# Performance work log

Hardware: AMD Instinct MI355X
Metric: run time of the kernel (lower is better)

Reference implementation:

```python
import jax, jax.numpy as jnp
import numpy as np
from jax import lax

B, M, D_IN, EPG = 512, 64, 32, 512   # pairs, nodes/graph, one_hot_dim, edges/graph
GCN_SIZES = [64, 32, 16]
K = 5                                 # conv kernel (odd -> 'same' pad 2)
LIN = [12288, 256, 64]                # 12288 = 3 sim-mats * 16 ch * 16 * 16


def _edges(seed):
    # random intra-graph edges: per-graph node ids in [0,M) offset by graph id
    r = np.random.default_rng(seed)
    off = np.repeat(np.arange(B, dtype=np.int64) * M, EPG)
    s = r.integers(0, M, B * EPG) + off
    d = r.integers(0, M, B * EPG) + off
    return jnp.asarray(s, jnp.int32), jnp.asarray(d, jnp.int32)


def setup_inputs():
    key = jax.random.key(0)
    ks = iter(jax.random.split(key, 32))
    def nrm(shape, fan_in):
        return jax.random.normal(next(ks), shape, jnp.float32) * (fan_in ** -0.5)
    src_q, dst_q = _edges(1)
    src_c, dst_c = _edges(2)
    return dict(
        x_q=jax.random.normal(next(ks), (B * M, D_IN), jnp.float32),
        x_c=jax.random.normal(next(ks), (B * M, D_IN), jnp.float32),
        src_q=src_q, dst_q=dst_q, src_c=src_c, dst_c=dst_c,
        Wg0=nrm((D_IN, 64), D_IN), bg0=jnp.zeros((64,), jnp.float32),
        Wg1=nrm((64, 32), 64), bg1=jnp.zeros((32,), jnp.float32),
        Wg2=nrm((32, 16), 32), bg2=jnp.zeros((16,), jnp.float32),
        cw0=nrm((3, 8, 1, K, K), K * K), cb0=jnp.zeros((3, 8), jnp.float32),
        cw1=nrm((3, 16, 8, K, K), 8 * K * K), cb1=jnp.zeros((3, 16), jnp.float32),
        Wl0=nrm((LIN[0], LIN[1]), LIN[0]), bl0=jnp.zeros((LIN[1],), jnp.float32),
        Wl1=nrm((LIN[1], LIN[2]), LIN[1]), bl1=jnp.zeros((LIN[2],), jnp.float32),
        Wsc=nrm((LIN[2], 1), LIN[2]), bsc=jnp.zeros((1,), jnp.float32),
    )


def _gcn_pass(x, src, dst, Ws, bs):
    # PyG GCNConv: x @ W, add self loops, symmetric deg^-1/2 normalization,
    # scatter-add to dst, + bias. Eval mode (dropout off).
    N = x.shape[0]
    sl = jnp.arange(N, dtype=src.dtype)
    s = jnp.concatenate([src, sl])
    d = jnp.concatenate([dst, sl])
    deg = jax.ops.segment_sum(jnp.ones(s.shape, x.dtype), d, num_segments=N)
    dinv = lax.rsqrt(deg)
    norm = (dinv[s] * dinv[d])[:, None]
    feats = []
    h = x
    for i in range(len(Ws)):
        h = h @ Ws[i]
        h = jax.ops.segment_sum(h[s] * norm, d, num_segments=N) + bs[i]
        feats.append(h)
        if i < len(Ws) - 1:
            h = jax.nn.relu(h)
    return feats


def _conv(x, w, b):
    y = lax.conv_general_dilated(x, w, (1, 1), ((K // 2, K // 2), (K // 2, K // 2)),
                                 dimension_numbers=('NCHW', 'OIHW', 'NCHW'))
    return y + b[None, :, None, None]


def _maxpool2(x):
    # torch: ZeroPad2d((0,1,0,1)) then MaxPool2d(2, 2)
    xp = jnp.pad(x, ((0, 0), (0, 0), (0, 1), (0, 1)))
    return lax.reduce_window(xp, -jnp.inf, lax.max, (1, 1, 2, 2), (1, 1, 2, 2), 'VALID')


def _forward(x_q, x_c, src_q, dst_q, src_c, dst_c,
             Wg0, bg0, Wg1, bg1, Wg2, bg2,
             cw0, cb0, cw1, cb1, Wl0, bl0, Wl1, bl1, Wsc, bsc):
    Ws, bs = [Wg0, Wg1, Wg2], [bg0, bg1, bg2]
    qf = _gcn_pass(x_q, src_q, dst_q, Ws, bs)
    cf = _gcn_pass(x_c, src_c, dst_c, Ws, bs)
    # all graphs have exactly M nodes -> pad_sequence is a reshape; sim is [B,1,M,M]
    feats = [jnp.einsum('bmd,bnd->bmn', qf[i].reshape(B, M, -1),
                        cf[i].reshape(B, M, -1))[:, None] for i in range(3)]
    cws, cbs = [cw0, cw1], [cb0, cb1]
    for l in range(2):
        feats = [_maxpool2(jax.nn.relu(_conv(feats[i], cws[l][i], cbs[l][i])))
                 for i in range(3)]
    h = jnp.concatenate(feats, axis=1).reshape(-1, LIN[0])
    h = jax.nn.relu(h @ Wl0 + bl0)
    h = jax.nn.relu(h @ Wl1 + bl1)
    return jax.nn.sigmoid(h @ Wsc + bsc).reshape(-1)


def reference(x_q, x_c, src_q, dst_q, src_c, dst_c,
              Wg0, bg0, Wg1, bg1, Wg2, bg2,
              cw0, cb0, cw1, cb1, Wl0, bl0, Wl1, bl1, Wsc, bsc):
    return _forward(x_q, x_c, src_q, dst_q, src_c, dst_c,
                    Wg0, bg0, Wg1, bg1, Wg2, bg2,
                    cw0, cb0, cw1, cb1, Wl0, bl0, Wl1, bl1, Wsc, bsc)
```

## Files before the change

kernel.cpp:

```cpp
#include <hip/hip_runtime.h>
#include <math.h>

#define NB 512
#define MM 64
#define EPGc 512

typedef __attribute__((ext_vector_type(8))) short s16x8;
typedef __attribute__((ext_vector_type(4))) float f32x4;

__device__ __forceinline__ unsigned short f2bf(float f) {
  union { float f; unsigned int u; } c; c.f = f;
  unsigned int u = c.u;
  return (unsigned short)((u + 0x7FFFu + ((u >> 16) & 1u)) >> 16);
}
__device__ __forceinline__ float bf2f(unsigned short h) {
  union { unsigned int u; float f; } c; c.u = ((unsigned int)h) << 16;
  return c.f;
}

template<int Fin, int Fout, bool RELU>
__device__ __forceinline__ void gcn_layer_mfma(
    const unsigned short* __restrict__ WT, const float* __restrict__ bias,
    unsigned short* hbuf, unsigned short* stT, const unsigned short* Ab,
    unsigned short* __restrict__ outG, int g, int tid)
{
  const int lane = tid & 63, w = tid >> 6;
  const int c = lane & 15, q = lane >> 4;
  constexpr int NT = Fout / 16;
  constexpr int KS = Fin / 32;

#pragma unroll
  for (int nt = 0; nt < NT; ++nt) {
    f32x4 acc = {0.f, 0.f, 0.f, 0.f};
#pragma unroll
    for (int ks = 0; ks < KS; ++ks) {
      s16x8 a = *reinterpret_cast<const s16x8*>(hbuf + (w * 16 + c) * 72 + ks * 32 + q * 8);
      s16x8 b = *reinterpret_cast<const s16x8*>(WT + (nt * 16 + c) * Fin + ks * 32 + q * 8);
      acc = __builtin_amdgcn_mfma_f32_16x16x32_bf16(a, b, acc, 0, 0, 0);
    }
    unsigned int w0 = (unsigned int)f2bf(acc[0]) | ((unsigned int)f2bf(acc[1]) << 16);
    unsigned int w1 = (unsigned int)f2bf(acc[2]) | ((unsigned int)f2bf(acc[3]) << 16);
    *reinterpret_cast<uint2*>(stT + (nt * 16 + c) * 72 + w * 16 + q * 4) = make_uint2(w0, w1);
  }
  __syncthreads();

#pragma unroll
  for (int mt = 0; mt < NT; ++mt) {
    f32x4 acc = {0.f, 0.f, 0.f, 0.f};
#pragma unroll
    for (int ks = 0; ks < 2; ++ks) {
      s16x8 a = *reinterpret_cast<const s16x8*>(stT + (mt * 16 + c) * 72 + ks * 32 + q * 8);
      s16x8 b = *reinterpret_cast<const s16x8*>(Ab + (w * 16 + c) * 72 + ks * 32 + q * 8);
      acc = __builtin_amdgcn_mfma_f32_16x16x32_bf16(a, b, acc, 0, 0, 0);
    }
    const int node = w * 16 + c, f0 = mt * 16 + q * 4;
    unsigned short pk[4], pr[4];
#pragma unroll
    for (int r = 0; r < 4; ++r) {
      float v = acc[r] + bias[f0 + r];
      pk[r] = f2bf(v);
      pr[r] = f2bf(fmaxf(v, 0.f));
    }
    *reinterpret_cast<uint2*>(outG + (size_t)(g * MM + node) * Fout + f0) =
        make_uint2((unsigned int)pk[0] | ((unsigned int)pk[1] << 16),
                   (unsigned int)pk[2] | ((unsigned int)pk[3] << 16));
    if (RELU)
      *reinterpret_cast<uint2*>(hbuf + node * 72 + f0) =
          make_uint2((unsigned int)pr[0] | ((unsigned int)pr[1] << 16),
                     (unsigned int)pr[2] | ((unsigned int)pr[3] << 16));
  }
  __syncthreads();
}

__global__ __launch_bounds__(256) void gcn_kernel(
    const float* __restrict__ xq, const float* __restrict__ xc,
    const int* __restrict__ srcq, const int* __restrict__ dstq,
    const int* __restrict__ srcc, const int* __restrict__ dstc,
    const unsigned short* __restrict__ WgT,
    const float* __restrict__ bg0, const float* __restrict__ bg1, const float* __restrict__ bg2,
    unsigned short* __restrict__ qf0, unsigned short* __restrict__ qf1,
    unsigned short* __restrict__ qf2, unsigned short* __restrict__ cf0,
    unsigned short* __restrict__ cf1, unsigned short* __restrict__ cf2)
{
  __shared__ __align__(16) unsigned short smem[13824];
  __shared__ float sDinv[MM];
  __shared__ int sDeg[MM];
  unsigned short* hbuf = smem;
  unsigned short* stT  = smem + 4608;
  unsigned short* Ab   = smem + 9216;
  float* sAf = reinterpret_cast<float*>(smem);

  const int g = blockIdx.x;
  const int which = blockIdx.y;
  const float* x = which ? xc : xq;
  const int* src = which ? srcc : srcq;
  const int* dst = which ? dstc : dstq;
  unsigned short* f0p = which ? cf0 : qf0;
  unsigned short* f1p = which ? cf1 : qf1;
  unsigned short* f2p = which ? cf2 : qf2;
  const int tid = threadIdx.x;

  for (int i = tid; i < 64 * 68; i += 256) sAf[i] = 0.f;
  if (tid < MM) sDeg[tid] = 1;
  __syncthreads();
  for (int e = tid; e < EPGc; e += 256)
    atomicAdd(&sDeg[dst[g * EPGc + e] - g * MM], 1);
  __syncthreads();
  if (tid < MM) sDinv[tid] = rsqrtf((float)sDeg[tid]);
  __syncthreads();
  for (int e = tid; e < EPGc; e += 256) {
    int s = src[g * EPGc + e] - g * MM;
    int d = dst[g * EPGc + e] - g * MM;
    atomicAdd(&sAf[d * 68 + s], sDinv[s] * sDinv[d]);
  }
  if (tid < MM) atomicAdd(&sAf[tid * 68 + tid], sDinv[tid] * sDinv[tid]);
  __syncthreads();
  for (int i = tid; i < 4096; i += 256) {
    int r = i >> 6, s = i & 63;
    Ab[r * 72 + s] = f2bf(sAf[r * 68 + s]);
  }
  __syncthreads();
  {
    const float* xs = x + (size_t)g * 2048 + tid * 8;
    float4 v0 = *reinterpret_cast<const float4*>(xs);
    float4 v1 = *reinterpret_cast<const float4*>(xs + 4);
    s16x8 p;
    p[0] = (short)f2bf(v0.x); p[1] = (short)f2bf(v0.y); p[2] = (short)f2bf(v0.z); p[3] = (short)f2bf(v0.w);
    p[4] = (short)f2bf(v1.x); p[5] = (short)f2bf(v1.y); p[6] = (short)f2bf(v1.z); p[7] = (short)f2bf(v1.w);
    int node = tid >> 2, k = (tid & 3) * 8;
    *reinterpret_cast<s16x8*>(hbuf + node * 72 + k) = p;
  }
  __syncthreads();

  gcn_layer_mfma<32, 64, true >(WgT,        bg0, hbuf, stT, Ab, f0p, g, tid);
  gcn_layer_mfma<64, 32, true >(WgT + 2048, bg1, hbuf, stT, Ab, f1p, g, tid);
  gcn_layer_mfma<32, 16, false>(WgT + 4096, bg2, hbuf, stT, Ab, f2p, g, tid);
}

__global__ __launch_bounds__(256) void prep_misc(
    const float* __restrict__ cw1, const float* __restrict__ cw0,
    const float* __restrict__ bl0,
    const float* __restrict__ Wg0, const float* __restrict__ Wg1, const float* __restrict__ Wg2,
    unsigned short* __restrict__ packA, unsigned short* __restrict__ packW1,
    unsigned short* __restrict__ WgT, float* __restrict__ l0)
{
  const int b = blockIdx.x, t = threadIdx.x;
  if (b < 512) {
    l0[b * 256 + t] = bl0[t];
    return;
  }
  if (b < 554) {
    int i = (b - 512) * 256 + t;
    if (i < 10752) {
      int j = i & 7, l = (i >> 3) & 63, g = (i >> 9) % 7, lvl = i / 3584;
      int oc = l & 15, sg = l >> 4;
      int s = g * 4 + sg;
      float v = 0.f;
      if (s < 25) v = cw1[((size_t)(lvl * 16 + oc) * 8 + j) * 25 + s];
      packA[i] = f2bf(v);
    }
    return;
  }
  if (b < 566) {
    int i = (b - 554) * 256 + t;
    if (i < 3072) {
      int j = i & 7, lane = (i >> 3) & 63, gg = (i >> 9) & 1, lvl = i >> 10;
      int m = lane & 15, q = lane >> 4;
      int u = gg * 4 + q;
      int oc = m & 7;
      float v = 0.f;
      if (u < 5) {
        if (m < 8) { if (j < 5) v = cw0[((size_t)(lvl * 8 + oc)) * 25 + u * 5 + j]; }
        else       { if (j >= 1 && j <= 5) v = cw0[((size_t)(lvl * 8 + oc)) * 25 + u * 5 + (j - 1)]; }
      }
      packW1[i] = f2bf(v);
    }
    return;
  }
  {
    int i = (b - 566) * 256 + t;
    if (i < 2048) {
      int n = i >> 5, k = i & 31;
      WgT[i] = f2bf(Wg0[k * 64 + n]);
    } else if (i < 4096) {
      int j = i - 2048, n = j >> 6, k = j & 63;
      WgT[i] = f2bf(Wg1[k * 32 + n]);
    } else if (i < 4608) {
      int j = i - 4096, n = j >> 5, k = j & 31;
      WgT[i] = f2bf(Wg2[k * 16 + n]);
    }
  }
}

__global__ __launch_bounds__(256) void pack_wl0(const float* __restrict__ Wl0,
                                                unsigned short* __restrict__ WT)
{
  __shared__ float tile[64][65];
  const int kb = blockIdx.x * 64;
  const int nb = blockIdx.y * 64;
  const int tid = threadIdx.x;
#pragma unroll
  for (int i = 0; i < 16; ++i) {
    int idx = i * 256 + tid, kk = idx >> 6, nn = idx & 63;
    tile[kk][nn] = Wl0[(size_t)(kb + kk) * 256 + nb + nn];
  }
  __syncthreads();
#pragma unroll
  for (int i = 0; i < 16; ++i) {
    int idx = i * 256 + tid, nn = idx >> 6, kk = idx & 63;
    WT[(size_t)(nb + nn) * 12288 + kb + kk] = f2bf(tile[kk][nn]);
  }
}

template<int F>
__device__ __forceinline__ void sim_mfma(const unsigned short* __restrict__ qf,
    const unsigned short* __restrict__ cf, unsigned short* qbf, unsigned short* cbf,
    unsigned short* cp, int g, int tid)
{
  constexpr int SQ = (F == 16) ? 40 : F + 8;
  {
    unsigned int* z = reinterpret_cast<unsigned int*>(cp);
    for (int i = tid; i < 2880; i += 256) z[i] = 0u;
  }
  for (int i = tid; i < 64 * F / 8; i += 256) {
    int row = (i * 8) / F, k = (i * 8) % F;
    s16x8 qv = *reinterpret_cast<const s16x8*>(qf + (size_t)g * 64 * F + i * 8);
    s16x8 cv = *reinterpret_cast<const s16x8*>(cf + (size_t)g * 64 * F + i * 8);
    *reinterpret_cast<s16x8*>(qbf + row * SQ + k) = qv;
    *reinterpret_cast<s16x8*>(cbf + row * SQ + k) = cv;
  }
  if (F == 16) {
    for (int i = tid; i < 128; i += 256) {
      int row = i >> 1, h = (i & 1) * 8;
      s16x8 zz = {0, 0, 0, 0, 0, 0, 0, 0};
      *reinterpret_cast<s16x8*>(qbf + row * SQ + 16 + h) = zz;
      *reinterpret_cast<s16x8*>(cbf + row * SQ + 16 + h) = zz;
    }
  }
  __syncthreads();

  const int lane = tid & 63, wave = tid >> 6;
  const int c = lane & 15, q = lane >> 4;
  constexpr int NK = (F == 64) ? 2 : 1;

  f32x4 acc[4];
#pragma unroll
  for (int nt = 0; nt < 4; ++nt) acc[nt] = (f32x4){0.f, 0.f, 0.f, 0.f};
#pragma unroll
  for (int ks = 0; ks < NK; ++ks) {
    s16x8 af = *reinterpret_cast<const s16x8*>(qbf + (wave * 16 + c) * SQ + ks * 32 + q * 8);
#pragma unroll
    for (int nt = 0; nt < 4; ++nt) {
      s16x8 bf = *reinterpret_cast<const s16x8*>(cbf + (nt * 16 + c) * SQ + ks * 32 + q * 8);
      acc[nt] = __builtin_amdgcn_mfma_f32_16x16x32_bf16(af, bf, acc[nt], 0, 0, 0);
    }
  }
#pragma unroll
  for (int nt = 0; nt < 4; ++nt)
#pragma unroll
    for (int r = 0; r < 4; ++r)
      cp[(wave * 16 + q * 4 + r + 2) * 80 + nt * 16 + c + 2] = f2bf(acc[nt][r]);
  __syncthreads();
}

__device__ __forceinline__ void conv1_mfma(const unsigned short* cp,
    unsigned short* p1u, const unsigned short* __restrict__ packW1,
    const float* __restrict__ cb0, int lvl, int tid)
{
  const int lane = tid & 63, wave = tid >> 6;
  const int c = lane & 15, q = lane >> 4;

  for (int h = tid; h < 272; h += 256) {
    int r, cc;
    if (h < 72)       { r = h / 36;             cc = h % 36; }
    else if (h < 144) { r = 34 + (h - 72) / 36; cc = (h - 72) % 36; }
    else { int z = h - 144; r = 2 + (z >> 2); int wq = z & 3; cc = (wq < 2) ? wq : 32 + wq; }
    s16x8 zz = {0, 0, 0, 0, 0, 0, 0, 0};
    *reinterpret_cast<s16x8*>(p1u + (r * 36 + cc) * 8) = zz;
  }

  s16x8 aw0 = *reinterpret_cast<const s16x8*>(packW1 + ((size_t)(lvl * 2 + 0) * 64 + lane) * 8);
  s16x8 aw1 = *reinterpret_cast<const s16x8*>(packW1 + ((size_t)(lvl * 2 + 1) * 64 + lane) * 8);
  float bias[4];
#pragma unroll
  for (int r = 0; r < 4; ++r) bias[r] = cb0[lvl * 8 + (q & 1) * 4 + r];

  const unsigned int* b32 = reinterpret_cast<const unsigned int*>(cp);

  for (int pp = 0; pp < 8; ++pp) {
    const int Y = wave * 8 + pp;
    const int y0 = 2 * Y;
#pragma unroll
    for (int Xi = 0; Xi < 2; ++Xi) {
      const int P = Xi * 16 + c;
      const int col = P;
      const int r00 = (y0 + q) * 40 + col;
      const int r01 = (y0 + 4 + q) * 40 + col;
      const int r10 = (y0 + 1 + q) * 40 + col;
      const int r11 = (y0 + 5 + q) * 40 + col;
      union { unsigned int w[4]; s16x8 v; } f00, f01, f10, f11;
#pragma unroll
      for (int k = 0; k < 4; ++k) {
        f00.w[k] = b32[r00 + k]; f01.w[k] = b32[r01 + k];
        f10.w[k] = b32[r10 + k]; f11.w[k] = b32[r11 + k];
      }
      f32x4 a0 = {0.f, 0.f, 0.f, 0.f}, a1 = {0.f, 0.f, 0.f, 0.f};
      a0 = __builtin_amdgcn_mfma_f32_16x16x32_bf16(aw0, f00.v, a0, 0, 0, 0);
      a0 = __builtin_amdgcn_mfma_f32_16x16x32_bf16(aw1, f01.v, a0, 0, 0, 0);
      a1 = __builtin_amdgcn_mfma_f32_16x16x32_bf16(aw0, f10.v, a1, 0, 0, 0);
      a1 = __builtin_amdgcn_mfma_f32_16x16x32_bf16(aw1, f11.v, a1, 0, 0, 0);
      float pv[4];
#pragma unroll
      for (int r = 0; r < 4; ++r) {
        float vm = fmaxf(a0[r], a1[r]);
        float hp = fmaxf(vm, __shfl_xor(vm, 32));
        pv[r] = fmaxf(hp + bias[r], 0.f);
      }
      if (q < 2) {
        unsigned short pk[4];
#pragma unroll
        for (int r = 0; r < 4; ++r) pk[r] = f2bf(pv[r]);
        unsigned int w0 = (unsigned int)pk[0] | ((unsigned int)pk[1] << 16);
        unsigned int w1 = (unsigned int)pk[2] | ((unsigned int)pk[3] << 16);
        *reinterpret_cast<uint2*>(p1u + (((Y + 2) * 36) + (P + 2)) * 8 + q * 4) =
            make_uint2(w0, w1);
      }
    }
  }
  __syncthreads();
}

__global__ __launch_bounds__(256) void simconv_kernel(
    const unsigned short* __restrict__ qf0, const unsigned short* __restrict__ qf1,
    const unsigned short* __restrict__ qf2, const unsigned short* __restrict__ cf0,
    const unsigned short* __restrict__ cf1, const unsigned short* __restrict__ cf2,
    const float* __restrict__ cb0, const float* __restrict__ cb1,
    const unsigned short* __restrict__ packA, const unsigned short* __restrict__ packW1,
    unsigned short* __restrict__ hcat)
{
  __shared__ __align__(16) unsigned short smem[16128];
  unsigned short* qbf = smem;
  unsigned short* cbf = smem + 4608;
  unsigned short* p1u = smem;
  unsigned short* cp  = smem + 10368;

  const int g = blockIdx.x, lvl = blockIdx.y, tid = threadIdx.x;

  if (lvl == 0)      sim_mfma<64>(qf0, cf0, qbf, cbf, cp, g, tid);
  else if (lvl == 1) sim_mfma<32>(qf1, cf1, qbf, cbf, cp, g, tid);
  else               sim_mfma<16>(qf2, cf2, qbf, cbf, cp, g, tid);

  conv1_mfma(cp, p1u, packW1, cb0, lvl, tid);

  {
    const int lane = tid & 63, wave = tid >> 6;
    const int col = lane & 15, q = lane >> 4;

    s16x8 afr[7];
#pragma unroll
    for (int gg = 0; gg < 7; ++gg)
      afr[gg] = *reinterpret_cast<const s16x8*>(packA + ((size_t)(lvl * 7 + gg) * 64 + lane) * 8);

    int off[7];
#pragma unroll
    for (int gg = 0; gg < 7; ++gg) {
      int s = gg * 4 + q; if (s > 24) s = 24;
      off[gg] = (s / 5) * 288 + (s % 5) * 8;
    }
    float bias2[4];
#pragma unroll
    for (int r = 0; r < 4; ++r) bias2[r] = cb1[lvl * 16 + q * 4 + r];

    for (int pq = 0; pq < 4; ++pq) {
      const int py = wave * 4 + pq;
#pragma unroll
      for (int h = 0; h < 2; ++h) {
        const int base0 = (2 * py) * 288 + h * 128 + col * 8;
        const int base1 = base0 + 288;
        f32x4 a0 = {0.f, 0.f, 0.f, 0.f}, a1 = {0.f, 0.f, 0.f, 0.f};
#pragma unroll
        for (int gg = 0; gg < 7; ++gg) {
          s16x8 b0 = *reinterpret_cast<const s16x8*>(p1u + base0 + off[gg]);
          a0 = __builtin_amdgcn_mfma_f32_16x16x32_bf16(afr[gg], b0, a0, 0, 0, 0);
          s16x8 b1 = *reinterpret_cast<const s16x8*>(p1u + base1 + off[gg]);
          a1 = __builtin_amdgcn_mfma_f32_16x16x32_bf16(afr[gg], b1, a1, 0, 0, 0);
        }
        float val[4];
#pragma unroll
        for (int r = 0; r < 4; ++r) {
          float vm = fmaxf(a0[r], a1[r]);
          float hp = fmaxf(vm, __shfl_xor(vm, 1));
          val[r] = fmaxf(hp + bias2[r], 0.f);
        }
        if ((col & 1) == 0) {
          int px = h * 8 + (col >> 1);
#pragma unroll
          for (int r = 0; r < 4; ++r)
            hcat[((size_t)g * 48 + lvl * 16 + q * 4 + r) * 256 + py * 16 + px] = f2bf(val[r]);
        }
      }
    }
  }
}

__global__ __launch_bounds__(256) void lin0_kernel(
    const unsigned short* __restrict__ A, const unsigned short* __restrict__ WT,
    float* __restrict__ l0)
{
  __shared__ __align__(16) unsigned short sAb[64 * 72];
  __shared__ __align__(16) unsigned short sBb[64 * 72];
  const int rb = blockIdx.x * 64;
  const int cb = blockIdx.y * 64;
  const int k0 = blockIdx.z * 768;
  const int tid = threadIdx.x;
  const int lane = tid & 63, wave = tid >> 6;
  const int wm = wave >> 1, wn = wave & 1;
  const int c = lane & 15, kg = lane >> 4;
  const int srow = tid >> 2;
  const int skq  = (tid & 3) * 16;

  f32x4 acc[2][2];
#pragma unroll
  for (int i = 0; i < 2; ++i)
#pragma unroll
    for (int j = 0; j < 2; ++j) acc[i][j] = (f32x4){0.f, 0.f, 0.f, 0.f};

  for (int kt = 0; kt < 768; kt += 64) {
    {
      const unsigned short* src = A + (size_t)(rb + srow) * 12288 + k0 + kt + skq;
      s16x8 a0 = *reinterpret_cast<const s16x8*>(src);
      s16x8 a1 = *reinterpret_cast<const s16x8*>(src + 8);
      *reinterpret_cast<s16x8*>(sAb + srow * 72 + skq)     = a0;
      *reinterpret_cast<s16x8*>(sAb + srow * 72 + skq + 8) = a1;
    }
    {
      const unsigned short* src = WT + (size_t)(cb + srow) * 12288 + k0 + kt + skq;
      s16x8 w0 = *reinterpret_cast<const s16x8*>(src);
      s16x8 w1 = *reinterpret_cast<const s16x8*>(src + 8);
      *reinterpret_cast<s16x8*>(sBb + srow * 72 + skq)     = w0;
      *reinterpret_cast<s16x8*>(sBb + srow * 72 + skq + 8) = w1;
    }
    __syncthreads();

#pragma unroll
    for (int kb = 0; kb < 64; kb += 32) {
      s16x8 a0 = *reinterpret_cast<const s16x8*>(sAb + (wm * 32 +  0 + c) * 72 + kb + kg * 8);
      s16x8 a1 = *reinterpret_cast<const s16x8*>(sAb + (wm * 32 + 16 + c) * 72 + kb + kg * 8);
      s16x8 b0 = *reinterpret_cast<const s16x8*>(sBb + (wn * 32 +  0 + c) * 72 + kb + kg * 8);
      s16x8 b1 = *reinterpret_cast<const s16x8*>(sBb + (wn * 32 + 16 + c) * 72 + kb + kg * 8);
      acc[0][0] = __builtin_amdgcn_mfma_f32_16x16x32_bf16(a0, b0, acc[0][0], 0, 0, 0);
      acc[0][1] = __builtin_amdgcn_mfma_f32_16x16x32_bf16(a0, b1, acc[0][1], 0, 0, 0);
      acc[1][0] = __builtin_amdgcn_mfma_f32_16x16x32_bf16(a1, b0, acc[1][0], 0, 0, 0);
      acc[1][1] = __builtin_amdgcn_mfma_f32_16x16x32_bf16(a1, b1, acc[1][1], 0, 0, 0);
    }
    __syncthreads();
  }

#pragma unroll
  for (int i = 0; i < 2; ++i)
#pragma unroll
    for (int j = 0; j < 2; ++j)
#pragma unroll
      for (int r = 0; r < 4; ++r) {
        int row = rb + wm * 32 + i * 16 + kg * 4 + r;
        int col = cb + wn * 32 + j * 16 + c;
        atomicAdd(&l0[(size_t)row * 256 + col], acc[i][j][r]);
      }
}

__global__ __launch_bounds__(64) void head_kernel(
    const float* __restrict__ l0, const float* __restrict__ Wl1, const float* __restrict__ bl1,
    const float* __restrict__ Wsc, const float* __restrict__ bsc, float* __restrict__ out)
{
  __shared__ float sr[256];
  const int b = blockIdx.x, j = threadIdx.x;
  for (int k = j; k < 256; k += 64) sr[k] = fmaxf(l0[(size_t)b * 256 + k], 0.f);
  __syncthreads();
  float acc = bl1[j];
  for (int k = 0; k < 256; ++k) acc = fmaf(sr[k], Wl1[k * 64 + j], acc);
  float v = fmaxf(acc, 0.f) * Wsc[j];
#pragma unroll
  for (int off = 32; off > 0; off >>= 1) v += __shfl_down(v, off);
  if (j == 0) out[b] = 1.f / (1.f + expf(-(v + bsc[0])));
}

extern "C" void kernel_launch(void* const* d_in, const int* in_sizes, int n_in,
                              void* d_out, int out_size, void* d_ws, size_t ws_size,
                              hipStream_t stream)
{
  (void)in_sizes; (void)n_in; (void)out_size; (void)ws_size;
  const float* x_q = (const float*)d_in[0];
  const float* x_c = (const float*)d_in[1];
  const int*   src_q = (const int*)d_in[2];
  const int*   dst_q = (const int*)d_in[3];
  const int*   src_c = (const int*)d_in[4];
  const int*   dst_c = (const int*)d_in[5];
  const float* Wg0 = (const float*)d_in[6];
  const float* bg0 = (const float*)d_in[7];
  const float* Wg1 = (const float*)d_in[8];
  const float* bg1 = (const float*)d_in[9];
  const float* Wg2 = (const float*)d_in[10];
  const float* bg2 = (const float*)d_in[11];
  const float* cw0 = (const float*)d_in[12];
  const float* cb0 = (const float*)d_in[13];
  const float* cw1 = (const float*)d_in[14];
  const float* cb1 = (const float*)d_in[15];
  const float* Wl0 = (const float*)d_in[16];
  const float* bl0 = (const float*)d_in[17];
  const float* Wl1 = (const float*)d_in[18];
  const float* bl1 = (const float*)d_in[19];
  const float* Wsc = (const float*)d_in[20];
  const float* bsc = (const float*)d_in[21];
  float* out = (float*)d_out;

  float* ws = (float*)d_ws;
  unsigned short* qf0 = (unsigned short*)ws; ws += (size_t)NB * MM * 64 / 2;
  unsigned short* qf1 = (unsigned short*)ws; ws += (size_t)NB * MM * 32 / 2;
  unsigned short* qf2 = (unsigned short*)ws; ws += (size_t)NB * MM * 16 / 2;
  unsigned short* cf0 = (unsigned short*)ws; ws += (size_t)NB * MM * 64 / 2;
  unsigned short* cf1 = (unsigned short*)ws; ws += (size_t)NB * MM * 32 / 2;
  unsigned short* cf2 = (unsigned short*)ws; ws += (size_t)NB * MM * 16 / 2;
  unsigned short* hcat = (unsigned short*)ws; ws += (size_t)NB * 48 * 256 / 2;
  float* l0  = ws; ws += (size_t)NB * 256;
  unsigned short* packA  = (unsigned short*)ws; ws += 5376;
  unsigned short* packW1 = (unsigned short*)ws; ws += 1536;
  unsigned short* WgT    = (unsigned short*)ws; ws += 2304;
  unsigned short* WT = (unsigned short*)ws; ws += (size_t)256 * 12288 / 2;

  prep_misc<<<584, 256, 0, stream>>>(cw1, cw0, bl0, Wg0, Wg1, Wg2, packA, packW1, WgT, l0);
  pack_wl0<<<dim3(192, 4), 256, 0, stream>>>(Wl0, WT);

  gcn_kernel<<<dim3(NB, 2), 256, 0, stream>>>(x_q, x_c, src_q, dst_q, src_c, dst_c,
      WgT, bg0, bg1, bg2, qf0, qf1, qf2, cf0, cf1, cf2);

  simconv_kernel<<<dim3(NB, 3), 256, 0, stream>>>(qf0, qf1, qf2, cf0, cf1, cf2,
      cb0, cb1, packA, packW1, hcat);

  lin0_kernel<<<dim3(8, 4, 16), 256, 0, stream>>>(hcat, WT, l0);
  head_kernel<<<NB, 64, 0, stream>>>(l0, Wl1, bl1, Wsc, bsc, out);
}
```

Measured before the change: 87.75 us.

## Replace lin0 atomic accumulation with split-K partial buffers reduced in head

```diff
diff --git a/kernel.cpp b/kernel.cpp
--- a/kernel.cpp
+++ b/kernel.cpp
@@ -139,18 +139,15 @@
 
 __global__ __launch_bounds__(256) void prep_misc(
     const float* __restrict__ cw1, const float* __restrict__ cw0,
-    const float* __restrict__ bl0,
     const float* __restrict__ Wg0, const float* __restrict__ Wg1, const float* __restrict__ Wg2,
+    const float* __restrict__ Wl0,
     unsigned short* __restrict__ packA, unsigned short* __restrict__ packW1,
-    unsigned short* __restrict__ WgT, float* __restrict__ l0)
-{
+    unsigned short* __restrict__ WgT, unsigned short* __restrict__ WT)
+{
+  __shared__ float tile[64][65];
   const int b = blockIdx.x, t = threadIdx.x;
-  if (b < 512) {
-    l0[b * 256 + t] = bl0[t];
-    return;
-  }
-  if (b < 554) {
-    int i = (b - 512) * 256 + t;
+  if (b < 42) {
+    int i = b * 256 + t;
     if (i < 10752) {
       int j = i & 7, l = (i >> 3) & 63, g = (i >> 9) % 7, lvl = i / 3584;
       int oc = l & 15, sg = l >> 4;
@@ -161,8 +158,8 @@
     }
     return;
   }
-  if (b < 566) {
-    int i = (b - 554) * 256 + t;
+  if (b < 54) {
+    int i = (b - 42) * 256 + t;
     if (i < 3072) {
       int j = i & 7, lane = (i >> 3) & 63, gg = (i >> 9) & 1, lvl = i >> 10;
       int m = lane & 15, q = lane >> 4;
@@ -177,8 +174,8 @@
     }
     return;
   }
-  {
-    int i = (b - 566) * 256 + t;
+  if (b < 72) {
+    int i = (b - 54) * 256 + t;
     if (i < 2048) {
       int n = i >> 5, k = i & 31;
       WgT[i] = f2bf(Wg0[k * 64 + n]);
@@ -189,26 +186,23 @@
       int j = i - 4096, n = j >> 5, k = j & 31;
       WgT[i] = f2bf(Wg2[k * 16 + n]);
     }
-  }
-}
-
-__global__ __launch_bounds__(256) void pack_wl0(const float* __restrict__ Wl0,
-                                                unsigned short* __restrict__ WT)
-{
-  __shared__ float tile[64][65];
-  const int kb = blockIdx.x * 64;
-  const int nb = blockIdx.y * 64;
-  const int tid = threadIdx.x;
-#pragma unroll
-  for (int i = 0; i < 16; ++i) {
-    int idx = i * 256 + tid, kk = idx >> 6, nn = idx & 63;
-    tile[kk][nn] = Wl0[(size_t)(kb + kk) * 256 + nb + nn];
-  }
-  __syncthreads();
-#pragma unroll
-  for (int i = 0; i < 16; ++i) {
-    int idx = i * 256 + tid, nn = idx >> 6, kk = idx & 63;
-    WT[(size_t)(nb + nn) * 12288 + kb + kk] = f2bf(tile[kk][nn]);
+    return;
+  }
+  {
+    int bb = b - 72;
+    const int kb = (bb % 192) * 64;
+    const int nb = (bb / 192) * 64;
+#pragma unroll
+    for (int i = 0; i < 16; ++i) {
+      int idx = i * 256 + t, kk = idx >> 6, nn = idx & 63;
+      tile[kk][nn] = Wl0[(size_t)(kb + kk) * 256 + nb + nn];
+    }
+    __syncthreads();
+#pragma unroll
+    for (int i = 0; i < 16; ++i) {
+      int idx = i * 256 + t, nn = idx >> 6, kk = idx & 63;
+      WT[(size_t)(nb + nn) * 12288 + kb + kk] = f2bf(tile[kk][nn]);
+    }
   }
 }
 
@@ -405,7 +399,7 @@
 
 __global__ __launch_bounds__(256) void lin0_kernel(
     const unsigned short* __restrict__ A, const unsigned short* __restrict__ WT,
-    float* __restrict__ l0)
+    float* __restrict__ part)
 {
   __shared__ __align__(16) unsigned short sAb[64 * 72];
   __shared__ __align__(16) unsigned short sBb[64 * 72];
@@ -456,6 +450,7 @@
     __syncthreads();
   }
 
+  float* dstp = part + (size_t)blockIdx.z * 512 * 256;
 #pragma unroll
   for (int i = 0; i < 2; ++i)
 #pragma unroll
@@ -464,17 +459,29 @@
       for (int r = 0; r < 4; ++r) {
         int row = rb + wm * 32 + i * 16 + kg * 4 + r;
         int col = cb + wn * 32 + j * 16 + c;
-        atomicAdd(&l0[(size_t)row * 256 + col], acc[i][j][r]);
+        dstp[(size_t)row * 256 + col] = acc[i][j][r];
       }
 }
 
 __global__ __launch_bounds__(64) void head_kernel(
-    const float* __restrict__ l0, const float* __restrict__ Wl1, const float* __restrict__ bl1,
+    const float* __restrict__ part, const float* __restrict__ bl0,
+    const float* __restrict__ Wl1, const float* __restrict__ bl1,
     const float* __restrict__ Wsc, const float* __restrict__ bsc, float* __restrict__ out)
 {
   __shared__ float sr[256];
   const int b = blockIdx.x, j = threadIdx.x;
-  for (int k = j; k < 256; k += 64) sr[k] = fmaxf(l0[(size_t)b * 256 + k], 0.f);
+  {
+    float4 s = *reinterpret_cast<const float4*>(bl0 + j * 4);
+#pragma unroll
+    for (int z = 0; z < 16; ++z) {
+      float4 p = *reinterpret_cast<const float4*>(part + ((size_t)z * 512 + b) * 256 + j * 4);
+      s.x += p.x; s.y += p.y; s.z += p.z; s.w += p.w;
+    }
+    sr[j * 4 + 0] = fmaxf(s.x, 0.f);
+    sr[j * 4 + 1] = fmaxf(s.y, 0.f);
+    sr[j * 4 + 2] = fmaxf(s.z, 0.f);
+    sr[j * 4 + 3] = fmaxf(s.w, 0.f);
+  }
   __syncthreads();
   float acc = bl1[j];
   for (int k = 0; k < 256; ++k) acc = fmaf(sr[k], Wl1[k * 64 + j], acc);
@@ -521,14 +528,14 @@
   unsigned short* cf1 = (unsigned short*)ws; ws += (size_t)NB * MM * 32 / 2;
   unsigned short* cf2 = (unsigned short*)ws; ws += (size_t)NB * MM * 16 / 2;
   unsigned short* hcat = (unsigned short*)ws; ws += (size_t)NB * 48 * 256 / 2;
-  float* l0  = ws; ws += (size_t)NB * 256;
+  float* part = ws; ws += (size_t)16 * 512 * 256;
   unsigned short* packA  = (unsigned short*)ws; ws += 5376;
   unsigned short* packW1 = (unsigned short*)ws; ws += 1536;
   unsigned short* WgT    = (unsigned short*)ws; ws += 2304;
   unsigned short* WT = (unsigned short*)ws; ws += (size_t)256 * 12288 / 2;
 
-  prep_misc<<<584, 256, 0, stream>>>(cw1, cw0, bl0, Wg0, Wg1, Wg2, packA, packW1, WgT, l0);
-  pack_wl0<<<dim3(192, 4), 256, 0, stream>>>(Wl0, WT);
+  prep_misc<<<840, 256, 0, stream>>>(cw1, cw0, Wg0, Wg1, Wg2, Wl0,
+                                     packA, packW1, WgT, WT);
 
   gcn_kernel<<<dim3(NB, 2), 256, 0, stream>>>(x_q, x_c, src_q, dst_q, src_c, dst_c,
       WgT, bg0, bg1, bg2, qf0, qf1, qf2, cf0, cf1, cf2);
@@ -536,6 +543,6 @@
   simconv_kernel<<<dim3(NB, 3), 256, 0, stream>>>(qf0, qf1, qf2, cf0, cf1, cf2,
       cb0, cb1, packA, packW1, hcat);
 
-  lin0_kernel<<<dim3(8, 4, 16), 256, 0, stream>>>(hcat, WT, l0);
-  head_kernel<<<NB, 64, 0, stream>>>(l0, Wl1, bl1, Wsc, bsc, out);
-}
+  lin0_kernel<<<dim3(8, 4, 16), 256, 0, stream>>>(hcat, WT, part);
+  head_kernel<<<NB, 64, 0, stream>>>(part, bl0, Wl1, bl1, Wsc, bsc, out);
+}
```

Result: faster. 78.68 us (median of 2 runs) (-10.3%).
